# Kernel optimization log

Measured on AMD Instinct MI355X. Metric: run time of the kernel, lower is better.

Reference implementation:

```python
import jax, jax.numpy as jnp
import numpy as np

NUM_EXPERTS = 4096
NUM_KEYS = 64  # floor(sqrt(num_experts))
TOP_K = 16
NORM_TOPK = False
BN_EPS = 1e-5


def setup_inputs() -> dict:
    key = jax.random.key(0)
    ks = jax.random.split(key, 7)
    B, S, H, I = 2, 2048, 2048, 8192
    s = 0.02
    return {
        "hidden_states": jax.random.normal(ks[0], (B, S, H), jnp.float32),
        "router_gate_w": jax.random.normal(ks[1], (2 * NUM_KEYS, H), jnp.float32) * s,
        "down_embed": jax.random.normal(ks[2], (NUM_EXPERTS, H), jnp.float32) * s,
        "up_embed": jax.random.normal(ks[3], (NUM_EXPERTS, H), jnp.float32) * s,
        "gate_w": jax.random.normal(ks[4], (I, H), jnp.float32) * s,
        "up_w": jax.random.normal(ks[5], (I, H), jnp.float32) * s,
        "down_w": jax.random.normal(ks[6], (H, I), jnp.float32) * s,
    }


def reference(hidden_states, router_gate_w, down_embed, up_embed, gate_w, up_w, down_w):
    B, S, H = hidden_states.shape
    x = hidden_states.reshape(-1, H)  # [N, H]

    # BatchNorm1d(affine=False), training-mode batch statistics (biased var)
    mu = jnp.mean(x, axis=0, keepdims=True)
    var = jnp.mean(jnp.square(x - mu), axis=0, keepdims=True)
    xn = (x - mu) * jax.lax.rsqrt(var + BN_EPS)

    # product-key router: logits [2, N, num_keys]
    rlog = (xn @ router_gate_w.T).reshape(-1, 2, NUM_KEYS).transpose(1, 0, 2)
    logp = jax.nn.log_softmax(rlog, axis=-1)

    # full product scores [N, nk, nk]; top-k over nk*nk candidates
    full = logp[0][:, :, None] + logp[1][:, None, :]
    scores, indices = jax.lax.top_k(full.reshape(-1, NUM_KEYS * NUM_KEYS), TOP_K)
    routing_weights = jnp.exp(scores)  # [N, k]
    if NORM_TOPK:
        routing_weights = routing_weights / jnp.sum(routing_weights, axis=-1, keepdims=True)

    # PEER-style expert: scalar key match then weighted up-embedding sum
    d = down_embed[indices]  # [N, k, H]
    u = up_embed[indices]    # [N, k, H]
    h = jnp.einsum('nh,nkh->nk', x, d)
    experts_states = jnp.einsum('nk,nk,nkh->nh', routing_weights, h, u)

    # dense gated MLP (silu)
    mlp = (jax.nn.silu(x @ gate_w.T) * (x @ up_w.T)) @ down_w.T

    out = (mlp + experts_states).reshape(B, S, H)
    return out, rlog
```

## Files before the change

### kernel.cpp

```cpp
#include <hip/hip_runtime.h>
#include <stdint.h>

#define H_DIM 2048
#define N_TOK 4096
#define I_DIM 8192

typedef __attribute__((ext_vector_type(8))) short short8;
typedef __attribute__((ext_vector_type(4))) float f32x4;

typedef const __attribute__((address_space(1))) unsigned int* gp_t;
typedef __attribute__((address_space(3))) unsigned int* lp_t;

__device__ __forceinline__ void gload16(const unsigned short* g, short* l) {
    __builtin_amdgcn_global_load_lds((gp_t)g, (lp_t)l, 16, 0, 0);
}

__device__ __forceinline__ unsigned short f2bf(float f) {
    union { float f; unsigned int u; } c; c.f = f;
    unsigned int u = c.u;
    return (unsigned short)((u + 0x7FFFu + ((u >> 16) & 1u)) >> 16);
}
__device__ __forceinline__ float bf2f(unsigned short u) {
    union { unsigned int i; float f; } c; c.i = ((unsigned int)u) << 16;
    return c.f;
}

__device__ __forceinline__ float wmax64(float v) {
#pragma unroll
    for (int o = 32; o > 0; o >>= 1) v = fmaxf(v, __shfl_xor(v, o));
    return v;
}
__device__ __forceinline__ float wsum64(float v) {
#pragma unroll
    for (int o = 32; o > 0; o >>= 1) v += __shfl_xor(v, o);
    return v;
}

template<int K, int RSTEP, int LSTEP>
__device__ __forceinline__ void stage4(const unsigned short* src, short* dst) {
#pragma unroll
    for (int j = 0; j < 4; ++j)
        gload16(src + (size_t)j * RSTEP * K, dst + j * LSTEP);
}
template<int K, int RSTEP, int LSTEP>
__device__ __forceinline__ void stage2(const unsigned short* src, short* dst) {
#pragma unroll
    for (int j = 0; j < 2; ++j)
        gload16(src + (size_t)j * RSTEP * K, dst + j * LSTEP);
}

__global__ __launch_bounds__(256) void bn_stats(const float* __restrict__ x,
                                                float* __restrict__ ps, float* __restrict__ pq) {
    int col = blockIdx.x * 256 + threadIdx.x;
    int r0  = blockIdx.y * 128;
    float s = 0.f, q = 0.f;
    for (int r = 0; r < 128; ++r) {
        float v = x[(size_t)(r0 + r) * H_DIM + col];
        s += v; q += v * v;
    }
    ps[blockIdx.y * H_DIM + col] = s;
    pq[blockIdx.y * H_DIM + col] = q;
}

__global__ __launch_bounds__(256) void bn_finalize(const float* __restrict__ ps, const float* __restrict__ pq,
                                                   float* __restrict__ mu, float* __restrict__ rsig) {
    int c = blockIdx.x * 256 + threadIdx.x;
    float s = 0.f, q = 0.f;
    for (int i = 0; i < 32; ++i) { s += ps[i * H_DIM + c]; q += pq[i * H_DIM + c]; }
    float m = s * (1.f / N_TOK);
    float v = q * (1.f / N_TOK) - m * m;
    mu[c] = m;
    rsig[c] = rsqrtf(v + 1e-5f);
}

__global__ __launch_bounds__(256) void cvt_all(const float* __restrict__ gw, const float* __restrict__ uw,
                                               const float* __restrict__ dw, const float* __restrict__ de,
                                               const float* __restrict__ ue, const float* __restrict__ x,
                                               unsigned short* __restrict__ gwb, unsigned short* __restrict__ uwb,
                                               unsigned short* __restrict__ dwb, unsigned short* __restrict__ deb,
                                               unsigned short* __restrict__ ueb, unsigned short* __restrict__ xb) {
    int b = blockIdx.x;
    const float* src; unsigned short* dst; size_t base;
    if      (b < 8192)  { src = gw; dst = gwb; base = (size_t)b; }
    else if (b < 16384) { src = uw; dst = uwb; base = (size_t)(b - 8192); }
    else if (b < 24576) { src = dw; dst = dwb; base = (size_t)(b - 16384); }
    else if (b < 28672) { src = de; dst = deb; base = (size_t)(b - 24576); }
    else if (b < 32768) { src = ue; dst = ueb; base = (size_t)(b - 28672); }
    else                { src = x;  dst = xb;  base = (size_t)(b - 32768); }
    size_t off = (base * 256 + threadIdx.x) * 8;
    float4 a = *(const float4*)(src + off);
    float4 c = *(const float4*)(src + off + 4);
    short8 s;
    s[0]=(short)f2bf(a.x); s[1]=(short)f2bf(a.y); s[2]=(short)f2bf(a.z); s[3]=(short)f2bf(a.w);
    s[4]=(short)f2bf(c.x); s[5]=(short)f2bf(c.y); s[6]=(short)f2bf(c.z); s[7]=(short)f2bf(c.w);
    *(short8*)(dst + off) = s;
}

__global__ __launch_bounds__(256) void cvt_x(const float* __restrict__ x, unsigned short* __restrict__ xb) {
    size_t i = ((size_t)blockIdx.x * 256 + threadIdx.x) * 4;
    float4 v = *(const float4*)(x + i);
    uint2 o;
    o.x = (unsigned)f2bf(v.x) | ((unsigned)f2bf(v.y) << 16);
    o.y = (unsigned)f2bf(v.z) | ((unsigned)f2bf(v.w) << 16);
    *(uint2*)(xb + i) = o;
}

__global__ __launch_bounds__(256) void cvt_w(const float* __restrict__ src, unsigned short* __restrict__ dst) {
    size_t off = ((size_t)blockIdx.x * 256 + threadIdx.x) * 8;
    float4 a = *(const float4*)(src + off);
    float4 b = *(const float4*)(src + off + 4);
    short8 s;
    s[0]=(short)f2bf(a.x); s[1]=(short)f2bf(a.y); s[2]=(short)f2bf(a.z); s[3]=(short)f2bf(a.w);
    s[4]=(short)f2bf(b.x); s[5]=(short)f2bf(b.y); s[6]=(short)f2bf(b.z); s[7]=(short)f2bf(b.w);
    *(short8*)(dst + off) = s;
}

__global__ __launch_bounds__(256) void router_kernel(const float* __restrict__ x, const float* __restrict__ rgw,
                                                     const float* __restrict__ mu, const float* __restrict__ rsig,
                                                     float* __restrict__ rlog) {
    __shared__ float xs[16][65];
    __shared__ float rs[128][65];
    const int t = threadIdx.x;
    const int n0 = blockIdx.x * 16;
    const int tk = t >> 5;
    const int jj = t & 31;
    float acc[2][4] = {{0.f,0.f,0.f,0.f},{0.f,0.f,0.f,0.f}};

    for (int kc = 0; kc < H_DIM; kc += 64) {
        {
            int row = t >> 4, c4 = (t & 15) * 4;
            float4 v = *(const float4*)(x + (size_t)(n0 + row) * H_DIM + kc + c4);
            float4 m = *(const float4*)(mu + kc + c4);
            float4 r = *(const float4*)(rsig + kc + c4);
            xs[row][c4 + 0] = (v.x - m.x) * r.x;
            xs[row][c4 + 1] = (v.y - m.y) * r.y;
            xs[row][c4 + 2] = (v.z - m.z) * r.z;
            xs[row][c4 + 3] = (v.w - m.w) * r.w;
        }
        {
            int row = t >> 1, base = (t & 1) * 32;
            const float* src = rgw + (size_t)row * H_DIM + kc + base;
#pragma unroll
            for (int i = 0; i < 8; ++i) {
                float4 v = *(const float4*)(src + i * 4);
                rs[row][base + i*4 + 0] = v.x;
                rs[row][base + i*4 + 1] = v.y;
                rs[row][base + i*4 + 2] = v.z;
                rs[row][base + i*4 + 3] = v.w;
            }
        }
        __syncthreads();
#pragma unroll 4
        for (int k = 0; k < 64; ++k) {
            float x0 = xs[tk][k], x1 = xs[tk + 8][k];
            float r0 = rs[jj][k], r1 = rs[jj + 32][k], r2 = rs[jj + 64][k], r3 = rs[jj + 96][k];
            acc[0][0] += x0 * r0; acc[0][1] += x0 * r1; acc[0][2] += x0 * r2; acc[0][3] += x0 * r3;
            acc[1][0] += x1 * r0; acc[1][1] += x1 * r1; acc[1][2] += x1 * r2; acc[1][3] += x1 * r3;
        }
        __syncthreads();
    }
#pragma unroll
    for (int a = 0; a < 2; ++a)
#pragma unroll
        for (int b = 0; b < 4; ++b) {
            int n = n0 + tk + 8 * a;
            int j = jj + 32 * b;
            rlog[(size_t)(j >> 6) * (N_TOK * 64) + (size_t)n * 64 + (j & 63)] = acc[a][b];
        }
}

__global__ __launch_bounds__(256) void topk_kernel(const float* __restrict__ rlog,
                                                   float* __restrict__ topw, int* __restrict__ topi) {
    const int lane = threadIdx.x & 63;
    const int n = blockIdx.x * 4 + (threadIdx.x >> 6);

    float a = rlog[(size_t)n * 64 + lane];
    float b = rlog[(size_t)(N_TOK * 64) + (size_t)n * 64 + lane];
    float ma = wmax64(a);
    float lpa = a - ma - logf(wsum64(expf(a - ma)));
    float mb = wmax64(b);
    float lpb = b - mb - logf(wsum64(expf(b - mb)));

    float va = lpa, vb = lpb;
    float tva = -1e30f, tvb = -1e30f; int tia = 0, tib = 0;
    for (int it = 0; it < 16; ++it) {
        float mx = wmax64(va);
        int w = __ffsll(__ballot(va == mx)) - 1;
        if (lane == it) { tva = mx; tia = w; }
        if (lane == w) va = -1e30f;
        mx = wmax64(vb);
        w = __ffsll(__ballot(vb == mx)) - 1;
        if (lane == it) { tvb = mx; tib = w; }
        if (lane == w) vb = -1e30f;
    }
    float av = __shfl(tva, lane >> 2);
    int   ai = __shfl(tia, lane >> 2);
    int   q0 = (lane & 3) * 4;
    float c0 = av + __shfl(tvb, q0 + 0); int b0 = __shfl(tib, q0 + 0);
    float c1 = av + __shfl(tvb, q0 + 1); int b1 = __shfl(tib, q0 + 1);
    float c2 = av + __shfl(tvb, q0 + 2); int b2 = __shfl(tib, q0 + 2);
    float c3 = av + __shfl(tvb, q0 + 3); int b3 = __shfl(tib, q0 + 3);

    for (int it = 0; it < 16; ++it) {
        float lv = c0; int lq = 0;
        if (c1 > lv) { lv = c1; lq = 1; }
        if (c2 > lv) { lv = c2; lq = 2; }
        if (c3 > lv) { lv = c3; lq = 3; }
        float mx = wmax64(lv);
        int w = __ffsll(__ballot(lv == mx)) - 1;
        if (lane == w) {
            int bj;
            switch (lq) {
                case 0:  bj = b0; c0 = -1e30f; break;
                case 1:  bj = b1; c1 = -1e30f; break;
                case 2:  bj = b2; c2 = -1e30f; break;
                default: bj = b3; c3 = -1e30f; break;
            }
            topw[n * 16 + it] = expf(mx);
            topi[n * 16 + it] = ai * 64 + bj;
        }
    }
}

__global__ __launch_bounds__(256) void experts_kernel_b(const float* __restrict__ x, const unsigned short* __restrict__ de,
                                                        const unsigned short* __restrict__ ue, const float* __restrict__ topw,
                                                        const int* __restrict__ topi, float* __restrict__ out) {
    __shared__ float psum[16][4];
    const int n = blockIdx.x;
    const int t = threadIdx.x, lane = t & 63, wid = t >> 6;

    float xr[8];
    {
        float4 v0 = *(const float4*)(x + (size_t)n * H_DIM + t * 8);
        float4 v1 = *(const float4*)(x + (size_t)n * H_DIM + t * 8 + 4);
        xr[0]=v0.x; xr[1]=v0.y; xr[2]=v0.z; xr[3]=v0.w;
        xr[4]=v1.x; xr[5]=v1.y; xr[6]=v1.z; xr[7]=v1.w;
    }
    int   eidx[16];
    float ew[16];
#pragma unroll
    for (int k = 0; k < 16; ++k) { eidx[k] = topi[n * 16 + k]; ew[k] = topw[n * 16 + k]; }

    short8 uf[8];
#pragma unroll
    for (int k = 0; k < 8; ++k)
        uf[k] = *(const short8*)(ue + (size_t)eidx[k] * H_DIM + t * 8);

#pragma unroll
    for (int k = 0; k < 16; ++k) {
        short8 d = *(const short8*)(de + (size_t)eidx[k] * H_DIM + t * 8);
        float p = 0.f;
#pragma unroll
        for (int j = 0; j < 8; ++j) p += bf2f((unsigned short)d[j]) * xr[j];
        p = wsum64(p);
        if (lane == 0) psum[k][wid] = p;
    }
    __syncthreads();

    float acc[8] = {0,0,0,0,0,0,0,0};
#pragma unroll
    for (int k = 0; k < 16; ++k) {
        float h = psum[k][0] + psum[k][1] + psum[k][2] + psum[k][3];
        float coef = ew[k] * h;
        short8 u = (k < 8) ? uf[k]
                           : *(const short8*)(ue + (size_t)eidx[k] * H_DIM + t * 8);
#pragma unroll
        for (int j = 0; j < 8; ++j) acc[j] += coef * bf2f((unsigned short)u[j]);
    }
    float4 o0 = {acc[0], acc[1], acc[2], acc[3]};
    float4 o1 = {acc[4], acc[5], acc[6], acc[7]};
    *(float4*)(out + (size_t)n * H_DIM + t * 8)     = o0;
    *(float4*)(out + (size_t)n * H_DIM + t * 8 + 4) = o1;
}

__global__ __launch_bounds__(256) void experts_kernel(const float* __restrict__ x, const float* __restrict__ de,
                                                      const float* __restrict__ ue, const float* __restrict__ topw,
                                                      const int* __restrict__ topi, float* __restrict__ out) {
    __shared__ float psum[16][4];
    const int n = blockIdx.x;
    const int t = threadIdx.x, lane = t & 63, wid = t >> 6;

    float xr[8];
    {
        float4 v0 = *(const float4*)(x + (size_t)n * H_DIM + t * 8);
        float4 v1 = *(const float4*)(x + (size_t)n * H_DIM + t * 8 + 4);
        xr[0]=v0.x; xr[1]=v0.y; xr[2]=v0.z; xr[3]=v0.w;
        xr[4]=v1.x; xr[5]=v1.y; xr[6]=v1.z; xr[7]=v1.w;
    }
    int   eidx[16];
    float ew[16];
#pragma unroll
    for (int k = 0; k < 16; ++k) { eidx[k] = topi[n * 16 + k]; ew[k] = topw[n * 16 + k]; }

#pragma unroll
    for (int k = 0; k < 16; ++k) {
        const float* dr = de + (size_t)eidx[k] * H_DIM + t * 8;
        float4 v0 = *(const float4*)dr;
        float4 v1 = *(const float4*)(dr + 4);
        float p = v0.x*xr[0] + v0.y*xr[1] + v0.z*xr[2] + v0.w*xr[3]
                + v1.x*xr[4] + v1.y*xr[5] + v1.z*xr[6] + v1.w*xr[7];
        p = wsum64(p);
        if (lane == 0) psum[k][wid] = p;
    }
    __syncthreads();

    float acc[8] = {0,0,0,0,0,0,0,0};
#pragma unroll
    for (int k = 0; k < 16; ++k) {
        float h = psum[k][0] + psum[k][1] + psum[k][2] + psum[k][3];
        float coef = ew[k] * h;
        const float* ur = ue + (size_t)eidx[k] * H_DIM + t * 8;
        float4 v0 = *(const float4*)ur;
        float4 v1 = *(const float4*)(ur + 4);
        acc[0] += coef * v0.x; acc[1] += coef * v0.y; acc[2] += coef * v0.z; acc[3] += coef * v0.w;
        acc[4] += coef * v1.x; acc[5] += coef * v1.y; acc[6] += coef * v1.z; acc[7] += coef * v1.w;
    }
    float4 o0 = {acc[0], acc[1], acc[2], acc[3]};
    float4 o1 = {acc[4], acc[5], acc[6], acc[7]};
    *(float4*)(out + (size_t)n * H_DIM + t * 8)     = o0;
    *(float4*)(out + (size_t)n * H_DIM + t * 8 + 4) = o1;
}

#define SWZB(row, byteoff) ((byteoff) ^ (((row) & 7) << 4))

#define NTGU (H_DIM / 64)

__global__ __launch_bounds__(512, 2) void gemm_gu256(const unsigned short* __restrict__ xb,
                                                     const unsigned short* __restrict__ gwb,
                                                     const unsigned short* __restrict__ uwb,
                                                     unsigned short* __restrict__ act) {
    __shared__ __attribute__((aligned(16))) short sA[2][16384];
    __shared__ __attribute__((aligned(16))) short sBg[2][8192];
    __shared__ __attribute__((aligned(16))) short sBu[2][8192];
    const int t = threadIdx.x;
    const int lane = t & 63, wid = t >> 6;
    const int wm = wid >> 1, wn = wid & 1;
    const int l15 = lane & 15, l4 = lane >> 4;
    const int bid = blockIdx.x;
    const int sw = (bid & 7) * 128 + (bid >> 3);
    const int bx = sw & 63, by = sw >> 6;
    const int row0 = by * 256, col0 = bx * 128;

    const int rseg = lane >> 3;
    const int chunk = (lane & 7) ^ rseg;
    const unsigned short* aSrc = xb  + (size_t)(row0 + wid * 8 + rseg) * H_DIM + chunk * 8;
    const unsigned short* gSrc = gwb + (size_t)(col0 + wid * 8 + rseg) * H_DIM + chunk * 8;
    const unsigned short* uSrc = uwb + (size_t)(col0 + wid * 8 + rseg) * H_DIM + chunk * 8;

    const int swzb = (l15 & 7) << 4;
    const int kx0 = (l4 * 16) ^ swzb;
    const int kx1 = (64 + l4 * 16) ^ swzb;
    const int arow = (wm * 64 + l15) * 64;
    const int brow = (wn * 64 + l15) * 64;

    f32x4 zero = {0.f, 0.f, 0.f, 0.f};
    f32x4 accg[4][4], accu[4][4];
#pragma unroll
    for (int m = 0; m < 4; ++m)
#pragma unroll
        for (int n = 0; n < 4; ++n) { accg[m][n] = zero; accu[m][n] = zero; }

    stage4<H_DIM, 64, 4096>(aSrc, &sA[0][wid * 512]);
    stage2<H_DIM, 64, 4096>(gSrc, &sBg[0][wid * 512]);
    stage2<H_DIM, 64, 4096>(uSrc, &sBu[0][wid * 512]);
    __syncthreads();

    int cur = 0;
    for (int g = 0; g < NTGU; ++g) {
        if (g + 1 < NTGU) {
            stage4<H_DIM, 64, 4096>(aSrc + (size_t)(g + 1) * 64, &sA[cur ^ 1][wid * 512]);
            stage2<H_DIM, 64, 4096>(gSrc + (size_t)(g + 1) * 64, &sBg[cur ^ 1][wid * 512]);
            stage2<H_DIM, 64, 4096>(uSrc + (size_t)(g + 1) * 64, &sBu[cur ^ 1][wid * 512]);
        }
        const short* Ac = &sA[cur][0];
        const short* Gc = &sBg[cur][0];
        const short* Uc = &sBu[cur][0];
        {
            short8 a0[4], bg0[4], bu0[4];
#pragma unroll
            for (int m = 0; m < 4; ++m) a0[m]  = *(const short8*)(Ac + arow + m * 1024 + (kx0 >> 1));
#pragma unroll
            for (int n = 0; n < 4; ++n) bg0[n] = *(const short8*)(Gc + brow + n * 1024 + (kx0 >> 1));
#pragma unroll
            for (int n = 0; n < 4; ++n) bu0[n] = *(const short8*)(Uc + brow + n * 1024 + (kx0 >> 1));
            __builtin_amdgcn_s_setprio(1);
#pragma unroll
            for (int m = 0; m < 4; ++m)
#pragma unroll
                for (int n = 0; n < 4; ++n) {
                    accg[m][n] = __builtin_amdgcn_mfma_f32_16x16x32_bf16(a0[m], bg0[n], accg[m][n], 0, 0, 0);
                    accu[m][n] = __builtin_amdgcn_mfma_f32_16x16x32_bf16(a0[m], bu0[n], accu[m][n], 0, 0, 0);
                }
            __builtin_amdgcn_s_setprio(0);
        }
        {
            short8 a1[4], bg1[4], bu1[4];
#pragma unroll
            for (int m = 0; m < 4; ++m) a1[m]  = *(const short8*)(Ac + arow + m * 1024 + (kx1 >> 1));
#pragma unroll
            for (int n = 0; n < 4; ++n) bg1[n] = *(const short8*)(Gc + brow + n * 1024 + (kx1 >> 1));
#pragma unroll
            for (int n = 0; n < 4; ++n) bu1[n] = *(const short8*)(Uc + brow + n * 1024 + (kx1 >> 1));
            __builtin_amdgcn_s_setprio(1);
#pragma unroll
            for (int m = 0; m < 4; ++m)
#pragma unroll
                for (int n = 0; n < 4; ++n) {
                    accg[m][n] = __builtin_amdgcn_mfma_f32_16x16x32_bf16(a1[m], bg1[n], accg[m][n], 0, 0, 0);
                    accu[m][n] = __builtin_amdgcn_mfma_f32_16x16x32_bf16(a1[m], bu1[n], accu[m][n], 0, 0, 0);
                }
            __builtin_amdgcn_s_setprio(0);
        }
        __syncthreads();
        cur ^= 1;
    }

    const int rbase = row0 + wm * 64, cbase = col0 + wn * 64;
#pragma unroll
    for (int m = 0; m < 4; ++m)
#pragma unroll
        for (int n = 0; n < 4; ++n)
#pragma unroll
            for (int j = 0; j < 4; ++j) {
                int r = rbase + m * 16 + l4 * 4 + j;
                int c2 = cbase + n * 16 + l15;
                float gv = accg[m][n][j];
                float uv = accu[m][n][j];
                float sv = gv / (1.f + expf(-gv));
                act[(size_t)r * I_DIM + c2] = f2bf(sv * uv);
            }
}

#define NTD (I_DIM / 64)

__global__ __launch_bounds__(256, 2) void gemm_down128(const unsigned short* __restrict__ act,
                                                       const unsigned short* __restrict__ dwb,
                                                       float* __restrict__ out) {
    __shared__ __attribute__((aligned(16))) short sA[2][8192];
    __shared__ __attribute__((aligned(16))) short sB[2][8192];
    const int t = threadIdx.x;
    const int lane = t & 63, wid = t >> 6;
    const int wm = wid >> 1, wn = wid & 1;
    const int l15 = lane & 15, l4 = lane >> 4;
    const int bid = blockIdx.x;
    const int sw = (bid & 7) * 64 + (bid >> 3);
    const int bx = sw & 15, by = sw >> 4;
    const int row0 = by * 128, col0 = bx * 128;

    const int rseg = lane >> 3;
    const int chunk = (lane & 7) ^ rseg;
    const unsigned short* aSrc = act + (size_t)(row0 + wid * 8 + rseg) * I_DIM + chunk * 8;
    const unsigned short* bSrc = dwb + (size_t)(col0 + wid * 8 + rseg) * I_DIM + chunk * 8;

    const int swzb = (l15 & 7) << 4;
    const int kx0 = (l4 * 16) ^ swzb;
    const int kx1 = (64 + l4 * 16) ^ swzb;
    const int arow = (wm * 64 + l15) * 64;
    const int brow = (wn * 64 + l15) * 64;

    f32x4 zero = {0.f, 0.f, 0.f, 0.f};
    f32x4 acc[4][4];
#pragma unroll
    for (int m = 0; m < 4; ++m)
#pragma unroll
        for (int n = 0; n < 4; ++n) acc[m][n] = zero;

    stage4<I_DIM, 32, 2048>(aSrc, &sA[0][wid * 512]);
    stage4<I_DIM, 32, 2048>(bSrc, &sB[0][wid * 512]);
    __syncthreads();

    int cur = 0;
    for (int g = 0; g < NTD; ++g) {
        if (g + 1 < NTD) {
            stage4<I_DIM, 32, 2048>(aSrc + (size_t)(g + 1) * 64, &sA[cur ^ 1][wid * 512]);
            stage4<I_DIM, 32, 2048>(bSrc + (size_t)(g + 1) * 64, &sB[cur ^ 1][wid * 512]);
        }
        const short* Ac = &sA[cur][0];
        const short* Bc = &sB[cur][0];
        {
            short8 a0[4], b0[4];
#pragma unroll
            for (int m = 0; m < 4; ++m) a0[m] = *(const short8*)(Ac + arow + m * 1024 + (kx0 >> 1));
#pragma unroll
            for (int n = 0; n < 4; ++n) b0[n] = *(const short8*)(Bc + brow + n * 1024 + (kx0 >> 1));
            __builtin_amdgcn_s_setprio(1);
#pragma unroll
            for (int m = 0; m < 4; ++m)
#pragma unroll
                for (int n = 0; n < 4; ++n)
                    acc[m][n] = __builtin_amdgcn_mfma_f32_16x16x32_bf16(a0[m], b0[n], acc[m][n], 0, 0, 0);
            __builtin_amdgcn_s_setprio(0);
        }
        {
            short8 a1[4], b1[4];
#pragma unroll
            for (int m = 0; m < 4; ++m) a1[m] = *(const short8*)(Ac + arow + m * 1024 + (kx1 >> 1));
#pragma unroll
            for (int n = 0; n < 4; ++n) b1[n] = *(const short8*)(Bc + brow + n * 1024 + (kx1 >> 1));
            __builtin_amdgcn_s_setprio(1);
#pragma unroll
            for (int m = 0; m < 4; ++m)
#pragma unroll
                for (int n = 0; n < 4; ++n)
                    acc[m][n] = __builtin_amdgcn_mfma_f32_16x16x32_bf16(a1[m], b1[n], acc[m][n], 0, 0, 0);
            __builtin_amdgcn_s_setprio(0);
        }
        __syncthreads();
        cur ^= 1;
    }

    const int rbase = row0 + wm * 64, cbase = col0 + wn * 64;
#pragma unroll
    for (int m = 0; m < 4; ++m)
#pragma unroll
        for (int n = 0; n < 4; ++n)
#pragma unroll
            for (int j = 0; j < 4; ++j) {
                int r = rbase + m * 16 + l4 * 4 + j;
                int c2 = cbase + n * 16 + l15;
                out[(size_t)r * H_DIM + c2] += acc[m][n][j];
            }
}

__global__ __launch_bounds__(256) void gemm_gu(const unsigned short* __restrict__ xb,
                                               const float* __restrict__ gw, const float* __restrict__ uw,
                                               unsigned short* __restrict__ act) {
    __shared__ __attribute__((aligned(16))) short As[128 * 64];
    __shared__ __attribute__((aligned(16))) short Bg[128 * 64];
    __shared__ __attribute__((aligned(16))) short Bu[128 * 64];
    const int t = threadIdx.x;
    const int lane = t & 63, wid = t >> 6;
    const int wr = wid >> 1, wc = wid & 1;
    const int l15 = lane & 15, l4 = lane >> 4;
    const int row0 = blockIdx.y * 128;
    const int col0 = blockIdx.x * 128;
    const int srow = t >> 1, shalf = (t & 1) * 32;

    f32x4 zero = {0.f, 0.f, 0.f, 0.f};
    f32x4 accg[4][4], accu[4][4];
#pragma unroll
    for (int m = 0; m < 4; ++m)
#pragma unroll
        for (int n = 0; n < 4; ++n) { accg[m][n] = zero; accu[m][n] = zero; }

    for (int kt = 0; kt < H_DIM; kt += 64) {
        {
            const unsigned short* src = xb + (size_t)(row0 + srow) * H_DIM + kt + shalf;
#pragma unroll
            for (int i = 0; i < 4; ++i) {
                int boff = SWZB(srow, (shalf + i * 8) * 2);
                *(short8*)(As + srow * 64 + (boff >> 1)) = *(const short8*)(src + i * 8);
            }
        }
        {
            const float* g = gw + (size_t)(col0 + srow) * H_DIM + kt + shalf;
            const float* u = uw + (size_t)(col0 + srow) * H_DIM + kt + shalf;
#pragma unroll
            for (int i = 0; i < 4; ++i) {
                int boff = SWZB(srow, (shalf + i * 8) * 2);
                float4 a0 = *(const float4*)(g + i * 8);
                float4 a1 = *(const float4*)(g + i * 8 + 4);
                short8 s;
                s[0]=(short)f2bf(a0.x); s[1]=(short)f2bf(a0.y); s[2]=(short)f2bf(a0.z); s[3]=(short)f2bf(a0.w);
                s[4]=(short)f2bf(a1.x); s[5]=(short)f2bf(a1.y); s[6]=(short)f2bf(a1.z); s[7]=(short)f2bf(a1.w);
                *(short8*)(Bg + srow * 64 + (boff >> 1)) = s;
                float4 b0 = *(const float4*)(u + i * 8);
                float4 b1 = *(const float4*)(u + i * 8 + 4);
                short8 r;
                r[0]=(short)f2bf(b0.x); r[1]=(short)f2bf(b0.y); r[2]=(short)f2bf(b0.z); r[3]=(short)f2bf(b0.w);
                r[4]=(short)f2bf(b1.x); r[5]=(short)f2bf(b1.y); r[6]=(short)f2bf(b1.z); r[7]=(short)f2bf(b1.w);
                *(short8*)(Bu + srow * 64 + (boff >> 1)) = r;
            }
        }
        __syncthreads();
#pragma unroll
        for (int kk = 0; kk < 64; kk += 32) {
            short8 af[4], bgf[4], buf_[4];
#pragma unroll
            for (int m = 0; m < 4; ++m) {
                int row = wr * 64 + m * 16 + l15;
                af[m] = *(const short8*)(As + row * 64 + (SWZB(row, (kk + l4 * 8) * 2) >> 1));
            }
#pragma unroll
            for (int n = 0; n < 4; ++n) {
                int row = wc * 64 + n * 16 + l15;
                int off = row * 64 + (SWZB(row, (kk + l4 * 8) * 2) >> 1);
                bgf[n]  = *(const short8*)(Bg + off);
                buf_[n] = *(const short8*)(Bu + off);
            }
#pragma unroll
            for (int m = 0; m < 4; ++m)
#pragma unroll
                for (int n = 0; n < 4; ++n) {
                    accg[m][n] = __builtin_amdgcn_mfma_f32_16x16x32_bf16(af[m], bgf[n],  accg[m][n], 0, 0, 0);
                    accu[m][n] = __builtin_amdgcn_mfma_f32_16x16x32_bf16(af[m], buf_[n], accu[m][n], 0, 0, 0);
                }
        }
        __syncthreads();
    }
    const int rbase = row0 + wr * 64, cbase = col0 + wc * 64;
#pragma unroll
    for (int m = 0; m < 4; ++m)
#pragma unroll
        for (int n = 0; n < 4; ++n)
#pragma unroll
            for (int j = 0; j < 4; ++j) {
                int r = rbase + m * 16 + l4 * 4 + j;
                int c = cbase + n * 16 + l15;
                float gv = accg[m][n][j];
                float uv = accu[m][n][j];
                float sv = gv / (1.f + expf(-gv));
                act[(size_t)r * I_DIM + c] = f2bf(sv * uv);
            }
}

__global__ __launch_bounds__(256) void gemm_down(const unsigned short* __restrict__ act,
                                                 const float* __restrict__ dw, float* __restrict__ out) {
    __shared__ __attribute__((aligned(16))) short As[128 * 64];
    __shared__ __attribute__((aligned(16))) short Bs[128 * 64];
    const int t = threadIdx.x;
    const int lane = t & 63, wid = t >> 6;
    const int wr = wid >> 1, wc = wid & 1;
    const int l15 = lane & 15, l4 = lane >> 4;
    const int row0 = blockIdx.y * 128;
    const int col0 = blockIdx.x * 128;
    const int srow = t >> 1, shalf = (t & 1) * 32;

    f32x4 zero = {0.f, 0.f, 0.f, 0.f};
    f32x4 acc[4][4];
#pragma unroll
    for (int m = 0; m < 4; ++m)
#pragma unroll
        for (int n = 0; n < 4; ++n) acc[m][n] = zero;

    for (int kt = 0; kt < I_DIM; kt += 64) {
        {
            const unsigned short* src = act + (size_t)(row0 + srow) * I_DIM + kt + shalf;
#pragma unroll
            for (int i = 0; i < 4; ++i) {
                int boff = SWZB(srow, (shalf + i * 8) * 2);
                *(short8*)(As + srow * 64 + (boff >> 1)) = *(const short8*)(src + i * 8);
            }
        }
        {
            const float* g = dw + (size_t)(col0 + srow) * I_DIM + kt + shalf;
#pragma unroll
            for (int i = 0; i < 4; ++i) {
                int boff = SWZB(srow, (shalf + i * 8) * 2);
                float4 a0 = *(const float4*)(g + i * 8);
                float4 a1 = *(const float4*)(g + i * 8 + 4);
                short8 s;
                s[0]=(short)f2bf(a0.x); s[1]=(short)f2bf(a0.y); s[2]=(short)f2bf(a0.z); s[3]=(short)f2bf(a0.w);
                s[4]=(short)f2bf(a1.x); s[5]=(short)f2bf(a1.y); s[6]=(short)f2bf(a1.z); s[7]=(short)f2bf(a1.w);
                *(short8*)(Bs + srow * 64 + (boff >> 1)) = s;
            }
        }
        __syncthreads();
#pragma unroll
        for (int kk = 0; kk < 64; kk += 32) {
            short8 af[4], bf[4];
#pragma unroll
            for (int m = 0; m < 4; ++m) {
                int row = wr * 64 + m * 16 + l15;
                af[m] = *(const short8*)(As + row * 64 + (SWZB(row, (kk + l4 * 8) * 2) >> 1));
            }
#pragma unroll
            for (int n = 0; n < 4; ++n) {
                int row = wc * 64 + n * 16 + l15;
                bf[n] = *(const short8*)(Bs + row * 64 + (SWZB(row, (kk + l4 * 8) * 2) >> 1));
            }
#pragma unroll
            for (int m = 0; m < 4; ++m)
#pragma unroll
                for (int n = 0; n < 4; ++n)
                    acc[m][n] = __builtin_amdgcn_mfma_f32_16x16x32_bf16(af[m], bf[n], acc[m][n], 0, 0, 0);
        }
        __syncthreads();
    }
    const int rbase = row0 + wr * 64, cbase = col0 + wc * 64;
#pragma unroll
    for (int m = 0; m < 4; ++m)
#pragma unroll
        for (int n = 0; n < 4; ++n)
#pragma unroll
            for (int j = 0; j < 4; ++j) {
                int r = rbase + m * 16 + l4 * 4 + j;
                int c = cbase + n * 16 + l15;
                out[(size_t)r * H_DIM + c] += acc[m][n][j];
            }
}

extern "C" void kernel_launch(void* const* d_in, const int* in_sizes, int n_in,
                              void* d_out, int out_size, void* d_ws, size_t ws_size,
                              hipStream_t stream) {
    const float* x   = (const float*)d_in[0];
    const float* rgw = (const float*)d_in[1];
    const float* de  = (const float*)d_in[2];
    const float* ue  = (const float*)d_in[3];
    const float* gw  = (const float*)d_in[4];
    const float* uw  = (const float*)d_in[5];
    const float* dw  = (const float*)d_in[6];
    float* out = (float*)d_out;
    char* ws = (char*)d_ws;

    float* ps   = (float*)(ws + 0);
    float* pq   = (float*)(ws + 262144);
    float* mu   = (float*)(ws + 524288);
    float* rsig = (float*)(ws + 532480);
    float* topw = (float*)(ws + 540672);
    int*   topi = (int*)  (ws + 802816);
    unsigned short* xb  = (unsigned short*)(ws + 1179648);
    unsigned short* act = (unsigned short*)(ws + 17956864);
    unsigned short* gwb = (unsigned short*)(ws + 85065728);
    unsigned short* uwb = (unsigned short*)(ws + 118620160);
    unsigned short* dwb = (unsigned short*)(ws + 152174592);
    unsigned short* deb = (unsigned short*)(ws + 185729024);
    unsigned short* ueb = (unsigned short*)(ws + 202506240);
    float* rlog = out + 8388608;
    const bool fast  = ws_size >= 185729024ULL;
    const bool fast2 = ws_size >= 219283456ULL;

    bn_stats   <<<dim3(8, 32), 256, 0, stream>>>(x, ps, pq);
    bn_finalize<<<8, 256, 0, stream>>>(ps, pq, mu, rsig);
    router_kernel<<<256, 256, 0, stream>>>(x, rgw, mu, rsig, rlog);
    topk_kernel<<<1024, 256, 0, stream>>>(rlog, topw, topi);

    if (fast2) {
        cvt_all<<<36864, 256, 0, stream>>>(gw, uw, dw, de, ue, x, gwb, uwb, dwb, deb, ueb, xb);
        experts_kernel_b<<<4096, 256, 0, stream>>>(x, deb, ueb, topw, topi, out);
        gemm_gu256<<<1024, 512, 0, stream>>>(xb, gwb, uwb, act);
        gemm_down128<<<512, 256, 0, stream>>>(act, dwb, out);
    } else if (fast) {
        cvt_x<<<8192, 256, 0, stream>>>(x, xb);
        cvt_w<<<8192, 256, 0, stream>>>(gw, gwb);
        cvt_w<<<8192, 256, 0, stream>>>(uw, uwb);
        cvt_w<<<8192, 256, 0, stream>>>(dw, dwb);
        experts_kernel<<<4096, 256, 0, stream>>>(x, de, ue, topw, topi, out);
        gemm_gu256<<<1024, 512, 0, stream>>>(xb, gwb, uwb, act);
        gemm_down128<<<512, 256, 0, stream>>>(act, dwb, out);
    } else {
        cvt_x<<<8192, 256, 0, stream>>>(x, xb);
        experts_kernel<<<4096, 256, 0, stream>>>(x, de, ue, topw, topi, out);
        gemm_gu  <<<dim3(64, 32), 256, 0, stream>>>(xb, gw, uw, act);
        gemm_down<<<dim3(16, 32), 256, 0, stream>>>(act, dw, out);
    }
}
```

Baseline: 760.5 us.

## Prefetch gate-weight tiles two stages ahead with partial vmcnt waits

Adds a third LDS buffer for the gate-weight tile and issues its global-to-LDS load two K-steps ahead, while the A and up-weight tiles stay double-buffered. The full __syncthreads is replaced by an explicit s_waitcnt vmcnt(2) plus s_barrier, so the newest gate prefetch can stay in flight across the barrier. The aim is to hide more global-load latency in the fused gate/up GEMM. The cost is extra LDS (16 KB more per block), which may threaten two-blocks-per-CU occupancy. The hand-counted vmcnt values also depend on how many loads stage2 and stage4 issue, so a miscount would be a correctness risk.

```diff
diff --git a/kernel.cpp b/kernel.cpp
--- a/kernel.cpp
+++ b/kernel.cpp
@@ -330,7 +330,7 @@
                                                      const unsigned short* __restrict__ uwb,
                                                      unsigned short* __restrict__ act) {
     __shared__ __attribute__((aligned(16))) short sA[2][16384];
-    __shared__ __attribute__((aligned(16))) short sBg[2][8192];
+    __shared__ __attribute__((aligned(16))) short sBg[3][8192];
     __shared__ __attribute__((aligned(16))) short sBu[2][8192];
     const int t = threadIdx.x;
     const int lane = t & 63, wid = t >> 6;
@@ -361,20 +361,32 @@
         for (int n = 0; n < 4; ++n) { accg[m][n] = zero; accu[m][n] = zero; }
 
     stage4<H_DIM, 64, 4096>(aSrc, &sA[0][wid * 512]);
+    stage2<H_DIM, 64, 4096>(uSrc, &sBu[0][wid * 512]);
     stage2<H_DIM, 64, 4096>(gSrc, &sBg[0][wid * 512]);
-    stage2<H_DIM, 64, 4096>(uSrc, &sBu[0][wid * 512]);
-    __syncthreads();
-
-    int cur = 0;
+    __builtin_amdgcn_sched_barrier(0);
+    stage2<H_DIM, 64, 4096>(gSrc + 64, &sBg[1][wid * 512]);
+    __builtin_amdgcn_sched_barrier(0);
+    asm volatile("s_waitcnt vmcnt(2)" ::: "memory");
+    __builtin_amdgcn_sched_barrier(0);
+    __builtin_amdgcn_s_barrier();
+    asm volatile("" ::: "memory");
+
     for (int g = 0; g < NTGU; ++g) {
+        const int ca = g & 1;
+        const int cg = g % 3;
         if (g + 1 < NTGU) {
-            stage4<H_DIM, 64, 4096>(aSrc + (size_t)(g + 1) * 64, &sA[cur ^ 1][wid * 512]);
-            stage2<H_DIM, 64, 4096>(gSrc + (size_t)(g + 1) * 64, &sBg[cur ^ 1][wid * 512]);
-            stage2<H_DIM, 64, 4096>(uSrc + (size_t)(g + 1) * 64, &sBu[cur ^ 1][wid * 512]);
-        }
-        const short* Ac = &sA[cur][0];
-        const short* Gc = &sBg[cur][0];
-        const short* Uc = &sBu[cur][0];
+            stage4<H_DIM, 64, 4096>(aSrc + (size_t)(g + 1) * 64, &sA[ca ^ 1][wid * 512]);
+            stage2<H_DIM, 64, 4096>(uSrc + (size_t)(g + 1) * 64, &sBu[ca ^ 1][wid * 512]);
+        }
+        __builtin_amdgcn_sched_barrier(0);
+        if (g + 2 < NTGU) {
+            stage2<H_DIM, 64, 4096>(gSrc + (size_t)(g + 2) * 64, &sBg[(g + 2) % 3][wid * 512]);
+        }
+        __builtin_amdgcn_sched_barrier(0);
+
+        const short* Ac = &sA[ca][0];
+        const short* Gc = &sBg[cg][0];
+        const short* Uc = &sBu[ca][0];
         {
             short8 a0[4], bg0[4], bu0[4];
 #pragma unroll
@@ -411,8 +423,12 @@
                 }
             __builtin_amdgcn_s_setprio(0);
         }
-        __syncthreads();
-        cur ^= 1;
+        __builtin_amdgcn_sched_barrier(0);
+        if (g + 2 < NTGU) { asm volatile("s_waitcnt vmcnt(2)" ::: "memory"); }
+        else              { asm volatile("s_waitcnt vmcnt(0)" ::: "memory"); }
+        __builtin_amdgcn_sched_barrier(0);
+        __builtin_amdgcn_s_barrier();
+        asm volatile("" ::: "memory");
     }
 
     const int rbase = row0 + wm * 64, cbase = col0 + wn * 64;
```

Measured after the change: 762.6 us. Within noise of the previous version (+0.3%).
